# Kernel tuning notes

Hardware: AMD Instinct MI355X
Metric: run time of the kernel (lower is better)

The kernel has to match this reference:

```python
import jax, jax.numpy as jnp
import numpy as np

N_NODES = 100000
N_EDGES = 1600000
IN_F = 128
HID = 128
N_CLASSES = 2
N_GRAPHS = 512


def setup_inputs() -> dict:
    key = jax.random.key(0)
    ks = jax.random.split(key, 12)
    x = jax.random.normal(ks[0], (N_NODES, IN_F), dtype=jnp.float32)
    edge_index = jax.random.randint(ks[1], (2, N_EDGES), 0, N_NODES, dtype=jnp.int64)
    batch = jnp.sort(jax.random.randint(ks[2], (N_NODES,), 0, N_GRAPHS, dtype=jnp.int64))
    s_in = 1.0 / np.sqrt(IN_F)
    s_h = 1.0 / np.sqrt(HID)
    return {
        "x": x,
        "edge_index": edge_index,
        "batch": batch,
        "W1": jax.random.normal(ks[3], (IN_F, HID), dtype=jnp.float32) * s_in,
        "b1": jnp.zeros((HID,), dtype=jnp.float32),
        "W2": jax.random.normal(ks[4], (HID, HID), dtype=jnp.float32) * s_h,
        "b2": jnp.zeros((HID,), dtype=jnp.float32),
        "W3": jax.random.normal(ks[5], (HID, HID), dtype=jnp.float32) * s_h,
        "b3": jnp.zeros((HID,), dtype=jnp.float32),
        "Wl": jax.random.normal(ks[6], (HID, N_CLASSES), dtype=jnp.float32) * s_h,
        "bl": jnp.zeros((N_CLASSES,), dtype=jnp.float32),
    }


def reference(x, edge_index, batch, W1, b1, W2, b2, W3, b3, Wl, bl):
    n = x.shape[0]
    src, dst = edge_index[0], edge_index[1]
    # GCNConv adds self-loops and applies symmetric normalization D^-1/2 (A+I) D^-1/2
    loop = jnp.arange(n, dtype=src.dtype)
    src_f = jnp.concatenate([src, loop])  # [E+N]
    dst_f = jnp.concatenate([dst, loop])
    deg = jax.ops.segment_sum(jnp.ones_like(src_f, dtype=x.dtype), dst_f, num_segments=n)
    dis = jax.lax.rsqrt(jnp.maximum(deg, 1.0))  # deg >= 1 due to self-loops
    norm = dis[src_f] * dis[dst_f]  # [E+N]

    def conv(h, W, b):
        h = h @ W                                    # [N, H]
        msg = h[src_f] * norm[:, None]               # gather + scale  [E+N, H]
        agg = jax.ops.segment_sum(msg, dst_f, num_segments=n)  # scatter-add
        return agg + b

    h = jax.nn.relu(conv(x, W1, b1))
    h = jax.nn.relu(conv(h, W2, b2))
    h = conv(h, W3, b3)
    # global_mean_pool over graph ids
    sums = jax.ops.segment_sum(h, batch, num_segments=N_GRAPHS)        # [G, H]
    cnt = jax.ops.segment_sum(jnp.ones((n,), h.dtype), batch, num_segments=N_GRAPHS)
    pooled = sums / jnp.maximum(cnt, 1.0)[:, None]
    # dropout p=0.5 is identity in eval mode
    return pooled @ Wl + bl
```

## Files before the change

kernel.cpp:

```cpp
#include <hip/hip_runtime.h>

#define NF 128
#define NFU 64
#define BW 128
#define KMAX 1024
#define CAP 3072
#define CHUNK 8192

typedef __attribute__((ext_vector_type(8))) short bf16x8;
typedef __attribute__((ext_vector_type(4))) float f32x4;
typedef __attribute__((ext_vector_type(2))) float f32x2;
union U4S8 { uint4 u; bf16x8 s; };

__global__ void detect_kernel(const int* __restrict__ ei, int ne, int* __restrict__ mode) {
    if (threadIdx.x == 0 && blockIdx.x == 0) {
        int step = ne / 32; if (step < 1) step = 1;
        int all0 = 1;
        for (int k = 0; k < 16; ++k) {
            int idx = 2 * k * step + 1;
            if (ei[idx] != 0) { all0 = 0; break; }
        }
        *mode = all0;
    }
}

__global__ __launch_bounds__(256) void hist_kernel(const int* __restrict__ ei, int ne, int n,
                                                   const int* __restrict__ mode, int* __restrict__ btotal,
                                                   int* __restrict__ blkcnt, int K) {
    __shared__ int hist[KMAX];
    int m = *mode;
    int tid = threadIdx.x;
    for (int k = tid; k < K; k += 256) hist[k] = 0;
    __syncthreads();
    int base = blockIdx.x * CHUNK;
    int end = min(base + CHUNK, ne);
    for (int e = base + tid; e < end; e += 256) {
        int dst = m ? ei[2 * (ne + e)] : ei[ne + e];
        if ((unsigned)dst < (unsigned)n) atomicAdd(&hist[dst >> 7], 1);
    }
    __syncthreads();
    for (int k = tid; k < K; k += 256) {
        int c = hist[k];
        blkcnt[(size_t)blockIdx.x * K + k] = c;
        if (c) atomicAdd(&btotal[k], c);
    }
}

__global__ __launch_bounds__(1024) void scanK(const int* __restrict__ btotal, int* __restrict__ bbase,
                                              int* __restrict__ gcur, int K) {
    __shared__ int sm[1024];
    int tid = threadIdx.x;
    int v = (tid < K) ? btotal[tid] : 0;
    sm[tid] = v;
    __syncthreads();
    for (int off = 1; off < 1024; off <<= 1) {
        int t = (tid >= off) ? sm[tid - off] : 0;
        __syncthreads();
        sm[tid] += t;
        __syncthreads();
    }
    if (tid < K) {
        int excl = sm[tid] - v;
        bbase[tid] = excl;
        gcur[tid] = excl;
        if (tid == K - 1) bbase[K] = sm[tid];
    }
}

__global__ __launch_bounds__(256) void scatter_kernel(const int* __restrict__ ei, int ne, int n,
                                                      const int* __restrict__ mode, const int* __restrict__ blkcnt,
                                                      int* __restrict__ gcur, unsigned* __restrict__ pairbuf,
                                                      int K) {
    __shared__ int cur[KMAX];
    int m = *mode;
    int tid = threadIdx.x;
    for (int k = tid; k < K; k += 256) {
        int c = blkcnt[(size_t)blockIdx.x * K + k];
        cur[k] = c ? atomicAdd(&gcur[k], c) : 0;
    }
    __syncthreads();
    int base = blockIdx.x * CHUNK;
    int end = min(base + CHUNK, ne);
    for (int e = base + tid; e < end; e += 256) {
        int src = m ? ei[2 * e] : ei[e];
        int dst = m ? ei[2 * (ne + e)] : ei[ne + e];
        if ((unsigned)dst >= (unsigned)n || (unsigned)src >= (unsigned)n) continue;
        int pos = atomicAdd(&cur[dst >> 7], 1);
        pairbuf[pos] = (unsigned)src | ((unsigned)(dst & (BW - 1)) << 24);
    }
}

__global__ __launch_bounds__(256) void sort_kernel(const unsigned* __restrict__ pairbuf,
                                                   const int* __restrict__ bbase,
                                                   int* __restrict__ rowptr, float* __restrict__ dis,
                                                   int* __restrict__ col, int n, int K) {
    __shared__ unsigned spair[CAP];
    __shared__ int lcol[CAP];
    __shared__ int dcnt[BW];
    __shared__ int pref[BW];
    int tid = threadIdx.x;
    int b = blockIdx.x;
    int r0 = b * BW;
    int base = bbase[b];
    int end = bbase[b + 1];
    int cntb = end - base;
    if (cntb > CAP) cntb = CAP;

    for (int i = tid; i < cntb; i += 256) spair[i] = pairbuf[base + i];
    if (tid < BW) dcnt[tid] = 0;
    __syncthreads();
    for (int i = tid; i < cntb; i += 256) atomicAdd(&dcnt[spair[i] >> 24], 1);
    __syncthreads();
    if (tid < BW) pref[tid] = dcnt[tid];
    __syncthreads();
    for (int off = 1; off < BW; off <<= 1) {
        int t = (tid < BW && tid >= off) ? pref[tid - off] : 0;
        __syncthreads();
        if (tid < BW) pref[tid] += t;
        __syncthreads();
    }
    if (tid < BW) {
        int d = r0 + tid;
        if (d < n) {
            int excl = pref[tid] - dcnt[tid];
            rowptr[d] = base + excl;
            dis[d] = rsqrtf((float)(dcnt[tid] + 1));
        }
    }
    if (b == K - 1 && tid == 0) rowptr[n] = end;
    if (tid < BW) dcnt[tid] = pref[tid] - dcnt[tid];
    __syncthreads();
    for (int i = tid; i < cntb; i += 256) {
        unsigned p = spair[i];
        int slot = atomicAdd(&dcnt[p >> 24], 1);
        if (slot < CAP) lcol[slot] = (int)(p & 0xFFFFFFu);
    }
    __syncthreads();
    for (int i = tid; i < cntb; i += 256) col[base + i] = lcol[i];
}

__device__ inline unsigned pack_bf16(float a, float b) {
    unsigned ua = __float_as_uint(a), ub = __float_as_uint(b);
    ua = (ua + 0x7fffu + ((ua >> 16) & 1u)) >> 16;
    ub = (ub + 0x7fffu + ((ub >> 16) & 1u)) >> 16;
    return ua | (ub << 16);
}
__device__ inline float bflo(unsigned u) { return __uint_as_float(u << 16); }
__device__ inline float bfhi(unsigned u) { return __uint_as_float(u & 0xFFFF0000u); }

__global__ __launch_bounds__(256) void wprep3_kernel(const float* __restrict__ W1, const float* __restrict__ W2,
                                                     const float* __restrict__ W3, uint4* __restrict__ Wb) {
    const float* W = (blockIdx.x == 0) ? W1 : (blockIdx.x == 1) ? W2 : W3;
    uint4* o = Wb + (size_t)blockIdx.x * 2048;
    int tid = threadIdx.x;
#pragma unroll
    for (int it = 0; it < 8; ++it) {
        int item = it * 256 + tid;
        int lane = item & 63;
        int kbjt = item >> 6;
        int kb = kbjt & 3, jt = kbjt >> 2;
        int k0 = kb * 32 + (lane >> 4) * 8;
        int j = jt * 16 + (lane & 15);
        unsigned p[4];
#pragma unroll
        for (int q = 0; q < 4; ++q)
            p[q] = pack_bf16(W[(size_t)(k0 + 2 * q) * NF + j], W[(size_t)(k0 + 2 * q + 1) * NF + j]);
        o[item] = make_uint4(p[0], p[1], p[2], p[3]);
    }
}

__global__ __launch_bounds__(256) void mm_mfma_kernel(const void* __restrict__ A, int a_fp32,
                                                      const uint4* __restrict__ Wb,
                                                      const float* __restrict__ dis,
                                                      unsigned* __restrict__ hs, int n) {
    int tid = threadIdx.x;
    int wave = tid >> 6, lane = tid & 63;
    int r0 = blockIdx.x * 64 + wave * 16;
    if (r0 >= n) return;
    int lrow = lane & 15, lk = lane >> 4;
    int arow = min(r0 + lrow, n - 1);

    f32x4 acc[8];
#pragma unroll
    for (int j = 0; j < 8; ++j) acc[j] = (f32x4){0.f, 0.f, 0.f, 0.f};

    U4S8 af[4];
    if (a_fp32) {
        const float* Af = (const float*)A;
#pragma unroll
        for (int kb = 0; kb < 4; ++kb) {
            const float* p = Af + (size_t)arow * NF + kb * 32 + lk * 8;
            float4 x0 = *(const float4*)p;
            float4 x1 = *(const float4*)(p + 4);
            af[kb].u = make_uint4(pack_bf16(x0.x, x0.y), pack_bf16(x0.z, x0.w),
                                  pack_bf16(x1.x, x1.y), pack_bf16(x1.z, x1.w));
        }
    } else {
        const unsigned* Ab = (const unsigned*)A;
#pragma unroll
        for (int kb = 0; kb < 4; ++kb)
            af[kb].u = *(const uint4*)(Ab + (size_t)arow * NFU + kb * 16 + lk * 4);
    }

#pragma unroll
    for (int kb = 0; kb < 4; ++kb) {
#pragma unroll
        for (int jt = 0; jt < 8; ++jt) {
            U4S8 wf;
            wf.u = Wb[(jt * 4 + kb) * 64 + lane];
            acc[jt] = __builtin_amdgcn_mfma_f32_16x16x32_bf16(wf.s, af[kb].s, acc[jt], 0, 0, 0);
        }
    }

    if (r0 + lrow < n) {
        float dv = dis[r0 + lrow];
        unsigned* orow = hs + (size_t)(r0 + lrow) * NFU;
#pragma unroll
        for (int jt = 0; jt < 8; ++jt) {
            unsigned p0 = pack_bf16(acc[jt][0] * dv, acc[jt][1] * dv);
            unsigned p1 = pack_bf16(acc[jt][2] * dv, acc[jt][3] * dv);
            *(uint2*)(orow + jt * 8 + lk * 2) = make_uint2(p0, p1);
        }
    }
}

#define SPACC(v)                                              \
    { a0 += (f32x2){bflo((v).x), bfhi((v).x)};                \
      a1 += (f32x2){bflo((v).y), bfhi((v).y)};                \
      a2 += (f32x2){bflo((v).z), bfhi((v).z)};                \
      a3 += (f32x2){bflo((v).w), bfhi((v).w)}; }

__global__ __launch_bounds__(256) void spmm_kernel(const unsigned* __restrict__ hs, const int* __restrict__ rowptr,
                                                   const int* __restrict__ col, const float* __restrict__ dis,
                                                   const float* __restrict__ b, unsigned* __restrict__ outb,
                                                   int n, int do_relu) {
    int wid = (blockIdx.x * blockDim.x + threadIdx.x) >> 6;
    int lane = threadIdx.x & 63;
    if (wid >= n) return;
    int s = rowptr[wid], e = rowptr[wid + 1];
    int deg = e - s;
    int group = lane >> 4, fl = lane & 15;

    f32x2 a0 = {0.f, 0.f}, a1 = {0.f, 0.f}, a2 = {0.f, 0.f}, a3 = {0.f, 0.f};
    if (group == 0) {
        uint4 sv = *(const uint4*)(hs + (size_t)wid * NFU + fl * 4);
        SPACC(sv);
    }

    int m64 = min(deg, 64);
    int cidx = (lane < m64) ? col[s + lane] : 0;

    int j0 = 0;
    for (; j0 + 8 <= m64; j0 += 8) {
        int ca = __shfl(cidx, j0 + group);
        int cb = __shfl(cidx, j0 + 4 + group);
        uint4 va = *(const uint4*)(hs + (size_t)ca * NFU + fl * 4);
        uint4 vb = *(const uint4*)(hs + (size_t)cb * NFU + fl * 4);
        SPACC(va);
        SPACC(vb);
    }
    for (; j0 < m64; j0 += 4) {
        int jj = j0 + group;
        int c = __shfl(cidx, jj);
        if (jj < m64) {
            uint4 v = *(const uint4*)(hs + (size_t)c * NFU + fl * 4);
            SPACC(v);
        }
    }
    for (int i = s + 64 + group; i < e; i += 4) {
        int c = col[i];
        uint4 v = *(const uint4*)(hs + (size_t)c * NFU + fl * 4);
        SPACC(v);
    }

#pragma unroll
    for (int k = 0; k < 2; ++k) {
        a0[k] += __shfl_xor(a0[k], 16); a0[k] += __shfl_xor(a0[k], 32);
        a1[k] += __shfl_xor(a1[k], 16); a1[k] += __shfl_xor(a1[k], 32);
        a2[k] += __shfl_xor(a2[k], 16); a2[k] += __shfl_xor(a2[k], 32);
        a3[k] += __shfl_xor(a3[k], 16); a3[k] += __shfl_xor(a3[k], 32);
    }

    if (lane < 16) {
        float d = dis[wid];
        float4 bb0 = *(const float4*)(b + fl * 8);
        float4 bb1 = *(const float4*)(b + fl * 8 + 4);
        float o[8];
        o[0] = fmaf(d, a0[0], bb0.x); o[1] = fmaf(d, a0[1], bb0.y);
        o[2] = fmaf(d, a1[0], bb0.z); o[3] = fmaf(d, a1[1], bb0.w);
        o[4] = fmaf(d, a2[0], bb1.x); o[5] = fmaf(d, a2[1], bb1.y);
        o[6] = fmaf(d, a3[0], bb1.z); o[7] = fmaf(d, a3[1], bb1.w);
        if (do_relu) {
#pragma unroll
            for (int k = 0; k < 8; ++k) o[k] = fmaxf(o[k], 0.f);
        }
        unsigned q0 = pack_bf16(o[0], o[1]);
        unsigned q1 = pack_bf16(o[2], o[3]);
        unsigned q2 = pack_bf16(o[4], o[5]);
        unsigned q3 = pack_bf16(o[6], o[7]);
        *(uint4*)(outb + (size_t)wid * NFU + fl * 4) = make_uint4(q0, q1, q2, q3);
    }
}

__global__ void gbounds_kernel(const int* __restrict__ batch, const int* __restrict__ mode,
                               int* __restrict__ gstart, int n, int G) {
    int m = *mode;
    int i = blockIdx.x * blockDim.x + threadIdx.x;
    if (i >= n) return;
    int g1 = m ? batch[2 * i] : batch[i];
    int g2 = (i == n - 1) ? G : (m ? batch[2 * (i + 1)] : batch[i + 1]);
    if ((unsigned)g1 > (unsigned)G) g1 = G;
    if ((unsigned)g2 > (unsigned)G) g2 = G;
    if (i == 0) for (int g = 0; g <= g1; ++g) gstart[g] = 0;
    for (int g = g1 + 1; g <= g2; ++g) gstart[g] = i + 1;
}

__global__ __launch_bounds__(256) void poolhead_kernel(const unsigned* __restrict__ h, const int* __restrict__ gstart,
                                                       const float* __restrict__ Wl, const float* __restrict__ bl,
                                                       float* __restrict__ out, int G) {
    __shared__ float sacc[16][16][8];
    int g = blockIdx.x >> 2, sub = blockIdx.x & 3;
    int s0 = gstart[g], e0 = gstart[g + 1];
    int cnt = e0 - s0;
    int per = (cnt + 3) >> 2;
    int s = s0 + sub * per;
    int e = min(s + per, e0);
    int tid = threadIdx.x;
    int rg = tid >> 4, fl = tid & 15;

    float acc[8] = {0.f, 0.f, 0.f, 0.f, 0.f, 0.f, 0.f, 0.f};
    for (int i = s + rg; i < e; i += 16) {
        uint4 v = *(const uint4*)(h + (size_t)i * NFU + fl * 4);
        acc[0] += bflo(v.x); acc[1] += bfhi(v.x);
        acc[2] += bflo(v.y); acc[3] += bfhi(v.y);
        acc[4] += bflo(v.z); acc[5] += bfhi(v.z);
        acc[6] += bflo(v.w); acc[7] += bfhi(v.w);
    }
#pragma unroll
    for (int k = 0; k < 8; ++k) sacc[rg][fl][k] = acc[k];
    __syncthreads();
    if (tid < 16) {
        float t[8] = {0.f, 0.f, 0.f, 0.f, 0.f, 0.f, 0.f, 0.f};
        for (int r = 0; r < 16; ++r)
#pragma unroll
            for (int k = 0; k < 8; ++k) t[k] += sacc[r][tid][k];
        float inv = 1.0f / fmaxf((float)cnt, 1.0f);
        float o0 = 0.f, o1 = 0.f;
#pragma unroll
        for (int k = 0; k < 8; ++k) {
            int f = tid * 8 + k;
            o0 += t[k] * inv * Wl[f * 2];
            o1 += t[k] * inv * Wl[f * 2 + 1];
        }
#pragma unroll
        for (int off2 = 8; off2; off2 >>= 1) {
            o0 += __shfl_down(o0, off2, 16);
            o1 += __shfl_down(o1, off2, 16);
        }
        if (tid == 0) {
            if (sub == 0) { o0 += bl[0]; o1 += bl[1]; }
            atomicAdd(&out[g * 2 + 0], o0);
            atomicAdd(&out[g * 2 + 1], o1);
        }
    }
}

extern "C" void kernel_launch(void* const* d_in, const int* in_sizes, int n_in,
                              void* d_out, int out_size, void* d_ws, size_t ws_size,
                              hipStream_t stream) {
    const float* x  = (const float*)d_in[0];
    const int*   ei = (const int*)d_in[1];
    const int*   bt = (const int*)d_in[2];
    const float* W1 = (const float*)d_in[3];
    const float* b1 = (const float*)d_in[4];
    const float* W2 = (const float*)d_in[5];
    const float* b2 = (const float*)d_in[6];
    const float* W3 = (const float*)d_in[7];
    const float* b3 = (const float*)d_in[8];
    const float* Wl = (const float*)d_in[9];
    const float* bl = (const float*)d_in[10];
    float* out = (float*)d_out;

    const int n  = in_sizes[2];
    const int ne = in_sizes[1] / 2;
    const int G  = out_size / 2;
    const int K  = (n + BW - 1) / BW;
    const int nchunks = (ne + CHUNK - 1) / CHUNK;

    size_t off = 0;
    auto alloc = [&](size_t bytes) { size_t o = off; off += (bytes + 255) & ~(size_t)255; return o; };
    char* ws = (char*)d_ws;
    unsigned* hB     = (unsigned*)(ws + alloc((size_t)n * NFU * 4));
    unsigned* hsB    = (unsigned*)(ws + alloc((size_t)n * NFU * 4));
    unsigned* pairbuf= (unsigned*)(ws + alloc((size_t)ne * 4));
    int*      col    = (int*)     (ws + alloc((size_t)ne * 4));
    int*      rowptr = (int*)     (ws + alloc((size_t)(n + 1) * 4));
    float*    dis    = (float*)   (ws + alloc((size_t)n * 4));
    int*      btotal = (int*)     (ws + alloc((size_t)(K + 1) * 4));
    int*      bbase  = (int*)     (ws + alloc((size_t)(K + 1) * 4));
    int*      gcur   = (int*)     (ws + alloc((size_t)(K + 1) * 4));
    int*      gstart = (int*)     (ws + alloc((size_t)(G + 1) * 4));
    int*      blkcnt = (int*)     (ws + alloc((size_t)nchunks * K * 4));
    uint4*    Wb     = (uint4*)   (ws + alloc(3 * 2048 * 16));
    int*      mode   = (int*)     (ws + alloc(256));
    (void)ws_size;

    hipMemsetAsync(btotal, 0, (size_t)(K + 1) * 4, stream);
    hipMemsetAsync(out, 0, (size_t)out_size * 4, stream);

    detect_kernel<<<1, 64, 0, stream>>>(ei, ne, mode);
    wprep3_kernel<<<3, 256, 0, stream>>>(W1, W2, W3, Wb);

    hist_kernel<<<nchunks, 256, 0, stream>>>(ei, ne, n, mode, btotal, blkcnt, K);
    scanK<<<1, 1024, 0, stream>>>(btotal, bbase, gcur, K);
    scatter_kernel<<<nchunks, 256, 0, stream>>>(ei, ne, n, mode, blkcnt, gcur, pairbuf, K);
    sort_kernel<<<K, 256, 0, stream>>>(pairbuf, bbase, rowptr, dis, col, n, K);
    gbounds_kernel<<<(n + 255) / 256, 256, 0, stream>>>(bt, mode, gstart, n, G);

    const int mm_grid = (n + 63) / 64;
    const int sp_grid = (n + 3) / 4;

    mm_mfma_kernel<<<mm_grid, 256, 0, stream>>>(x, 1, Wb, dis, hsB, n);
    spmm_kernel<<<sp_grid, 256, 0, stream>>>(hsB, rowptr, col, dis, b1, hB, n, 1);
    mm_mfma_kernel<<<mm_grid, 256, 0, stream>>>(hB, 0, Wb + 2048, dis, hsB, n);
    spmm_kernel<<<sp_grid, 256, 0, stream>>>(hsB, rowptr, col, dis, b2, hB, n, 1);
    mm_mfma_kernel<<<mm_grid, 256, 0, stream>>>(hB, 0, Wb + 4096, dis, hsB, n);
    spmm_kernel<<<sp_grid, 256, 0, stream>>>(hsB, rowptr, col, dis, b3, hB, n, 0);

    poolhead_kernel<<<G * 4, 256, 0, stream>>>(hB, gstart, Wl, bl, out, G);
}
```

Measured before the change: 321.3 us.

## Assign one 16-lane group per row in SpMM instead of a full wavefront

The SpMM kernel now processes four rows per wavefront, one per 16-lane group, instead of one row per 64-lane wavefront split into four edge groups. This removes the cross-group shuffle reduction and the idle lanes in the epilogue, and gives every lane useful work for the average degree of about 17. In exchange, each row's edges are walked serially by one group, so high-degree rows cause divergence within a wavefront and there is less memory-level parallelism per row.

```diff
diff --git a/kernel.cpp b/kernel.cpp
--- a/kernel.cpp
+++ b/kernel.cpp
@@ -234,72 +234,56 @@
                                                    const int* __restrict__ col, const float* __restrict__ dis,
                                                    const float* __restrict__ b, unsigned* __restrict__ outb,
                                                    int n, int do_relu) {
-    int wid = (blockIdx.x * blockDim.x + threadIdx.x) >> 6;
-    int lane = threadIdx.x & 63;
-    if (wid >= n) return;
-    int s = rowptr[wid], e = rowptr[wid + 1];
+    int row = (blockIdx.x * blockDim.x + threadIdx.x) >> 4;
+    int fl = threadIdx.x & 15;
+    int gbase = threadIdx.x & 48;
+    if (row >= n) return;
+    int s = rowptr[row], e = rowptr[row + 1];
     int deg = e - s;
-    int group = lane >> 4, fl = lane & 15;
-
-    f32x2 a0 = {0.f, 0.f}, a1 = {0.f, 0.f}, a2 = {0.f, 0.f}, a3 = {0.f, 0.f};
-    if (group == 0) {
-        uint4 sv = *(const uint4*)(hs + (size_t)wid * NFU + fl * 4);
-        SPACC(sv);
-    }
-
-    int m64 = min(deg, 64);
-    int cidx = (lane < m64) ? col[s + lane] : 0;
-
-    int j0 = 0;
-    for (; j0 + 8 <= m64; j0 += 8) {
-        int ca = __shfl(cidx, j0 + group);
-        int cb = __shfl(cidx, j0 + 4 + group);
-        uint4 va = *(const uint4*)(hs + (size_t)ca * NFU + fl * 4);
-        uint4 vb = *(const uint4*)(hs + (size_t)cb * NFU + fl * 4);
-        SPACC(va);
-        SPACC(vb);
-    }
-    for (; j0 < m64; j0 += 4) {
-        int jj = j0 + group;
-        int c = __shfl(cidx, jj);
-        if (jj < m64) {
-            uint4 v = *(const uint4*)(hs + (size_t)c * NFU + fl * 4);
-            SPACC(v);
-        }
-    }
-    for (int i = s + 64 + group; i < e; i += 4) {
-        int c = col[i];
-        uint4 v = *(const uint4*)(hs + (size_t)c * NFU + fl * 4);
-        SPACC(v);
-    }
-
-#pragma unroll
-    for (int k = 0; k < 2; ++k) {
-        a0[k] += __shfl_xor(a0[k], 16); a0[k] += __shfl_xor(a0[k], 32);
-        a1[k] += __shfl_xor(a1[k], 16); a1[k] += __shfl_xor(a1[k], 32);
-        a2[k] += __shfl_xor(a2[k], 16); a2[k] += __shfl_xor(a2[k], 32);
-        a3[k] += __shfl_xor(a3[k], 16); a3[k] += __shfl_xor(a3[k], 32);
-    }
-
-    if (lane < 16) {
-        float d = dis[wid];
-        float4 bb0 = *(const float4*)(b + fl * 8);
-        float4 bb1 = *(const float4*)(b + fl * 8 + 4);
-        float o[8];
-        o[0] = fmaf(d, a0[0], bb0.x); o[1] = fmaf(d, a0[1], bb0.y);
-        o[2] = fmaf(d, a1[0], bb0.z); o[3] = fmaf(d, a1[1], bb0.w);
-        o[4] = fmaf(d, a2[0], bb1.x); o[5] = fmaf(d, a2[1], bb1.y);
-        o[6] = fmaf(d, a3[0], bb1.z); o[7] = fmaf(d, a3[1], bb1.w);
-        if (do_relu) {
-#pragma unroll
-            for (int k = 0; k < 8; ++k) o[k] = fmaxf(o[k], 0.f);
-        }
-        unsigned q0 = pack_bf16(o[0], o[1]);
-        unsigned q1 = pack_bf16(o[2], o[3]);
-        unsigned q2 = pack_bf16(o[4], o[5]);
-        unsigned q3 = pack_bf16(o[6], o[7]);
-        *(uint4*)(outb + (size_t)wid * NFU + fl * 4) = make_uint4(q0, q1, q2, q3);
-    }
+
+    const unsigned* hsf = hs + fl * 4;
+    uint4 sv = *(const uint4*)(hsf + (size_t)row * NFU);
+    f32x2 a0 = {bflo(sv.x), bfhi(sv.x)};
+    f32x2 a1 = {bflo(sv.y), bfhi(sv.y)};
+    f32x2 a2 = {bflo(sv.z), bfhi(sv.z)};
+    f32x2 a3 = {bflo(sv.w), bfhi(sv.w)};
+
+    for (int jb = 0; jb < deg; jb += 16) {
+        int m = min(16, deg - jb);
+        int cidx = col[s + jb + ((fl < m) ? fl : (m - 1))];
+        int j = 0;
+        for (; j + 2 <= m; j += 2) {
+            int c0 = __shfl(cidx, gbase + j);
+            int c1 = __shfl(cidx, gbase + j + 1);
+            uint4 v0 = *(const uint4*)(hsf + (size_t)c0 * NFU);
+            uint4 v1 = *(const uint4*)(hsf + (size_t)c1 * NFU);
+            SPACC(v0);
+            SPACC(v1);
+        }
+        if (j < m) {
+            int c0 = __shfl(cidx, gbase + j);
+            uint4 v0 = *(const uint4*)(hsf + (size_t)c0 * NFU);
+            SPACC(v0);
+        }
+    }
+
+    float d = dis[row];
+    float4 bb0 = *(const float4*)(b + fl * 8);
+    float4 bb1 = *(const float4*)(b + fl * 8 + 4);
+    float o[8];
+    o[0] = fmaf(d, a0[0], bb0.x); o[1] = fmaf(d, a0[1], bb0.y);
+    o[2] = fmaf(d, a1[0], bb0.z); o[3] = fmaf(d, a1[1], bb0.w);
+    o[4] = fmaf(d, a2[0], bb1.x); o[5] = fmaf(d, a2[1], bb1.y);
+    o[6] = fmaf(d, a3[0], bb1.z); o[7] = fmaf(d, a3[1], bb1.w);
+    if (do_relu) {
+#pragma unroll
+        for (int k = 0; k < 8; ++k) o[k] = fmaxf(o[k], 0.f);
+    }
+    unsigned q0 = pack_bf16(o[0], o[1]);
+    unsigned q1 = pack_bf16(o[2], o[3]);
+    unsigned q2 = pack_bf16(o[4], o[5]);
+    unsigned q3 = pack_bf16(o[6], o[7]);
+    *(uint4*)(outb + (size_t)row * NFU + fl * 4) = make_uint4(q0, q1, q2, q3);
 }
 
 __global__ void gbounds_kernel(const int* __restrict__ batch, const int* __restrict__ mode,
@@ -418,7 +402,7 @@
     gbounds_kernel<<<(n + 255) / 256, 256, 0, stream>>>(bt, mode, gstart, n, G);
 
     const int mm_grid = (n + 63) / 64;
-    const int sp_grid = (n + 3) / 4;
+    const int sp_grid = (n + 15) / 16;
 
     mm_mfma_kernel<<<mm_grid, 256, 0, stream>>>(x, 1, Wb, dis, hsB, n);
     spmm_kernel<<<sp_grid, 256, 0, stream>>>(hsB, rowptr, col, dis, b1, hB, n, 1);
```

Result: no change. 320.8 us (-0.2%).
